# Kernel tuning notes

Hardware: AMD Instinct MI355X
Metric: run time of the kernel (lower is better)

The kernel has to match this reference:

```python
import jax, jax.numpy as jnp
import numpy as np

B = 8192
K = 40          # history blocks of 61
STATS = 383     # 99 base + 120 + 10 + 150 + 4 option dims
D = 165 + 61 * K + STATS  # 2988


def _mha(q, k, v, kpm, w_in, b_in, w_out, b_out, nh=4):
    """PyTorch nn.MultiheadAttention (batch_first) math. kpm: True = masked key."""
    Bq, Lq, E = q.shape
    hd = E // nh
    wq, wk, wv = jnp.split(w_in, 3, axis=0)
    bq, bk, bv = jnp.split(b_in, 3)
    qh = (q @ wq.T + bq).reshape(Bq, Lq, nh, hd).transpose(0, 2, 1, 3)
    kh = (k @ wk.T + bk).reshape(Bq, -1, nh, hd).transpose(0, 2, 1, 3)
    vh = (v @ wv.T + bv).reshape(Bq, -1, nh, hd).transpose(0, 2, 1, 3)
    s = jnp.einsum('bhqd,bhkd->bhqk', qh, kh) * jnp.float32(1.0 / np.sqrt(hd))
    if kpm is not None:
        s = jnp.where(kpm[:, None, None, :], jnp.float32(-1e9), s)
    a = jax.nn.softmax(s, axis=-1)
    o = jnp.einsum('bhqk,bhkd->bhqd', a, vh).transpose(0, 2, 1, 3).reshape(Bq, Lq, E)
    return o @ w_out.T + b_out


def _ln(x, g, b, eps=1e-5):
    m = x.mean(-1, keepdims=True)
    v = ((x - m) ** 2).mean(-1, keepdims=True)
    return (x - m) / jnp.sqrt(v + eps) * g + b


def setup_inputs() -> dict:
    key = jax.random.key(0)
    ks = iter(jax.random.split(key, 64))
    def p(shape, scale=0.02):
        return jax.random.normal(next(ks), shape, dtype=jnp.float32) * scale
    return {
        'obs': jax.random.normal(next(ks), (B, D), dtype=jnp.float32),
        'seat_team_vec': jax.random.normal(next(ks), (B, 6), dtype=jnp.float32),
        'card_emb': p((40, 32)),
        'w_cnt_hand': p((16, 3)), 'b_cnt_hand': p((16,)),
        'w_cnt_cap': p((16, 2)), 'b_cnt_cap': p((16,)),
        'h2t_win': p((96, 32)), 'h2t_bin': p((96,)), 'h2t_wout': p((32, 32)), 'h2t_bout': p((32,)),
        't2h_win': p((96, 32)), 't2h_bin': p((96,)), 't2h_wout': p((32, 32)), 't2h_bout': p((32,)),
        'w_merge': p((64, 224)), 'b_merge': p((64,)),
        'w_hproj': p((64, 61)), 'b_hproj': p((64,)),
        'pos_emb': p((40, 64)),
        'enc_win': p((192, 64)), 'enc_bin': p((192,)), 'enc_wout': p((64, 64)), 'enc_bout': p((64,)),
        'ln1_g': jnp.ones((64,), jnp.float32), 'ln1_b': jnp.zeros((64,), jnp.float32),
        'w_ff1': p((128, 64)), 'b_ff1': p((128,)),
        'w_ff2': p((64, 128)), 'b_ff2': p((64,)),
        'ln2_g': jnp.ones((64,), jnp.float32), 'ln2_b': jnp.zeros((64,), jnp.float32),
        'w_stats': p((64, STATS)), 'b_stats': p((64,)),
        'w_seat': p((32, 6)), 'b_seat': p((32,)),
        'w_comb': p((256, 224)), 'b_comb': p((256,)),
    }


def reference(obs, seat_team_vec, card_emb, w_cnt_hand, b_cnt_hand, w_cnt_cap, b_cnt_cap,
              h2t_win, h2t_bin, h2t_wout, h2t_bout, t2h_win, t2h_bin, t2h_wout, t2h_bout,
              w_merge, b_merge, w_hproj, b_hproj, pos_emb,
              enc_win, enc_bin, enc_wout, enc_bout, ln1_g, ln1_b,
              w_ff1, b_ff1, w_ff2, b_ff2, ln2_g, ln2_b,
              w_stats, b_stats, w_seat, b_seat, w_comb, b_comb):
    Bn = obs.shape[0]
    k = K  # static: decoded from D = 165 + 61*K + STATS
    hand_table = obs[:, :83]
    captured = obs[:, 83:165]
    history = obs[:, 165:165 + 61 * k]
    stats = obs[:, 165 + 61 * k:]

    hand_mask = hand_table[:, :40]
    other_counts = hand_table[:, 40:43]
    table_mask = hand_table[:, 43:83]

    hand_feat = hand_mask @ card_emb      # [B,32]
    table_feat = table_mask @ card_emb
    other_cnt_feat = jax.nn.relu(other_counts @ w_cnt_hand.T + b_cnt_hand)

    hand_present = hand_mask > 0.5
    table_present = table_mask > 0.5
    hand_seq = hand_mask[:, :, None] * card_emb    # [B,40,32]
    table_seq = table_mask[:, :, None] * card_emb

    # _safe_mha: rows whose keys are all padded produce zeros
    h2t = _mha(hand_seq, table_seq, table_seq, ~table_present, h2t_win, h2t_bin, h2t_wout, h2t_bout)
    h2t = jnp.where(table_present.any(axis=1)[:, None, None], h2t, jnp.float32(0.0))
    t2h = _mha(table_seq, hand_seq, hand_seq, ~hand_present, t2h_win, t2h_bin, t2h_wout, t2h_bout)
    t2h = jnp.where(hand_present.any(axis=1)[:, None, None], t2h, jnp.float32(0.0))

    def masked_mean(x, present):
        m = present[:, :, None].astype(x.dtype)
        return (x * m).sum(1) / jnp.maximum(m.sum(1), 1.0)
    hand_attn_feat = masked_mean(h2t, hand_present)
    table_attn_feat = masked_mean(t2h, table_present)

    cap0_feat = captured[:, :40] @ card_emb
    cap1_feat = captured[:, 40:80] @ card_emb
    cap_cnt_feat = jax.nn.relu(captured[:, 80:82] @ w_cnt_cap.T + b_cnt_cap)

    set_merged = jnp.concatenate([hand_feat, table_feat, cap0_feat, cap1_feat,
                                  hand_attn_feat, table_attn_feat,
                                  other_cnt_feat, cap_cnt_feat], axis=1)  # [B,224]
    set_feat = jax.nn.relu(set_merged @ w_merge.T + b_merge)              # [B,64]

    # 1-layer post-norm TransformerEncoder (eval mode, no dropout)
    hseq = history.reshape(Bn, k, 61) @ w_hproj.T + b_hproj + pos_emb[:k]  # [B,k,64]
    sa = _mha(hseq, hseq, hseq, None, enc_win, enc_bin, enc_wout, enc_bout)
    x = _ln(hseq + sa, ln1_g, ln1_b)
    ff = jax.nn.relu(x @ w_ff1.T + b_ff1) @ w_ff2.T + b_ff2
    x = _ln(x + ff, ln2_g, ln2_b)
    hist_feat = x.mean(axis=1)                                            # [B,64]

    stats_feat = jax.nn.relu(stats @ w_stats.T + b_stats)                 # [B,64]
    seat_feat = jax.nn.relu(seat_team_vec @ w_seat.T + b_seat)            # [B,32]

    combined = jnp.concatenate([set_feat, hist_feat, stats_feat, seat_feat], axis=1)  # [B,224]
    return jax.nn.relu(combined @ w_comb.T + b_comb)                      # [B,256]
```

## Files before the change

### kernel.cpp

```cpp
#include <hip/hip_runtime.h>

#define TPB 512

#define OFF_CV      0
#define OFF_POSB    2560
#define OFF_G       3840
#define OFF_U       10240
#define OFF_V       10560
#define OFF_CTB     10880
#define OFF_FRHP    10888
#define OFF_FRAG    14984
#define FR_QKV      0
#define FR_OUT      12288
#define FR_FF1      16384
#define FR_FF2      24576
#define OFF_MERGE   47752
#define OFF_STATS   62088
#define OFF_COMB    86600
#define OFF_WO2     143944
#define WS_TOTAL    144968

#define SA_OFF    0
#define HISTH_OFF 10240
#define HISTL_OFF 16768
#define QPL_OFF   10240
#define KF_OFF    16384
#define KZ_OFF    22528
#define OH_OFF    10240
#define FF1P_OFF  10240
#define C_OFF     23296
#define DH_OFF    33536
#define DL_OFF    40448
#define S_OFF     33536
#define SHT_OFF   47360
#define SOM_OFF   48032
#define SSM_OFF   48288
#define SCB_OFF   49184
#define R12_OFF   50208
#define SCNT_OFF  52256
#define SMEM_BYTES 52264

typedef __attribute__((ext_vector_type(8))) short bf16x8;
typedef __attribute__((ext_vector_type(4))) float f32x4;

struct P {
  const float *obs, *seat, *ce, *wch, *bch, *wcc, *bcc,
    *h2t_win, *h2t_bin, *h2t_wout, *h2t_bout,
    *t2h_win, *t2h_bin, *t2h_wout, *t2h_bout,
    *w_merge, *b_merge, *w_hproj, *b_hproj, *pos,
    *enc_win, *enc_bin, *enc_wout, *enc_bout,
    *ln1_g, *ln1_b, *w_ff1, *b_ff1, *w_ff2, *b_ff2, *ln2_g, *ln2_b,
    *w_stats, *b_stats, *w_seat, *b_seat, *w_comb, *b_comb;
  const float* ws;
  float* out;
};

__device__ __host__ inline unsigned bfpack(float a, float b, int plane) {
  unsigned ua = __float_as_uint(a) & 0xFFFF0000u;
  unsigned ub = __float_as_uint(b) & 0xFFFF0000u;
  if (plane == 0) return (ua >> 16) | ub;
  float ra = a - __uint_as_float(ua), rb = b - __uint_as_float(ub);
  return (__float_as_uint(ra) >> 16) | (__float_as_uint(rb) & 0xFFFF0000u);
}

__device__ inline unsigned short bf16rne(float x) {
  unsigned u = __float_as_uint(x);
  return (unsigned short)((u + 0x7FFFu + ((u >> 16) & 1u)) >> 16);
}

__device__ inline unsigned packrne(float a, float b) {
  return (unsigned)bf16rne(a) | ((unsigned)bf16rne(b) << 16);
}

__device__ inline float bf_lo(unsigned u) { return __uint_as_float(u << 16); }
__device__ inline float bf_hi(unsigned u) { return __uint_as_float(u & 0xFFFF0000u); }

__device__ inline bf16x8 ld_b64x2(const char* pp) {
  bf16x8 v;
  *((uint2*)&v) = *(const uint2*)(pp);
  *(((uint2*)&v) + 1) = *(const uint2*)(pp + 8);
  return v;
}

#define CSCALE 0.35355339059327373f

__global__ void prep_kernel(P p, float* ws) {
  int t = blockIdx.x * blockDim.x + threadIdx.x;
  if (t >= WS_TOTAL) return;
  unsigned* wsu = (unsigned*)ws;
  if (t < OFF_POSB) {
    int a = t / 1280, rem = t - a * 1280;
    int i = rem >> 5, d = rem & 31;
    const float* win = a ? p.t2h_win : p.h2t_win;
    const float* wr = win + (64 + d) * 32;
    const float* cr = p.ce + i * 32;
    float acc = 0.f;
    #pragma unroll
    for (int j = 0; j < 32; ++j) acc += cr[j] * wr[j];
    ws[t] = acc;
  } else if (t < OFF_G) {
    int r = t - OFF_POSB; int i = r >> 5, u = r & 31;
    float a = p.b_hproj[2 * u] + p.pos[i * 64 + 2 * u];
    float b = p.b_hproj[2 * u + 1] + p.pos[i * 64 + 2 * u + 1];
    wsu[t] = packrne(a, b);
  } else if (t < OFF_U) {
    int r = t - OFF_G;
    int u = r % 20; int i = (r / 20) % 40; int h = (r / 800) & 3; int a = r / 3200;
    const float* win = a ? p.t2h_win : p.h2t_win;
    const float* cri = p.ce + i * 32;
    float g2[2];
    #pragma unroll
    for (int half = 0; half < 2; ++half) {
      int j = 2 * u + half;
      const float* crj = p.ce + j * 32;
      float g = 0.f;
      for (int e = 0; e < 8; ++e) {
        const float* wq = win + (h * 8 + e) * 32;
        const float* wk = win + (32 + h * 8 + e) * 32;
        float pq = 0.f, pk = 0.f;
        for (int m = 0; m < 32; ++m) { pq += cri[m] * wq[m]; pk += crj[m] * wk[m]; }
        g += pq * pk;
      }
      g2[half] = g * CSCALE;
    }
    wsu[t] = packrne(g2[0], g2[1]);
  } else if (t < OFF_V) {
    int r = t - OFF_U; int i = r % 40; int h = (r / 40) & 3; int a = r / 160;
    const float* win = a ? p.t2h_win : p.h2t_win;
    const float* bin = a ? p.t2h_bin : p.h2t_bin;
    const float* cri = p.ce + i * 32;
    float u = 0.f;
    for (int e = 0; e < 8; ++e) {
      const float* wq = win + (h * 8 + e) * 32;
      float pq = 0.f;
      for (int m = 0; m < 32; ++m) pq += cri[m] * wq[m];
      u += pq * bin[32 + h * 8 + e];
    }
    ws[t] = u * CSCALE;
  } else if (t < OFF_CTB) {
    int r = t - OFF_V; int j = r % 40; int h = (r / 40) & 3; int a = r / 160;
    const float* win = a ? p.t2h_win : p.h2t_win;
    const float* bin = a ? p.t2h_bin : p.h2t_bin;
    const float* crj = p.ce + j * 32;
    float v = 0.f;
    for (int e = 0; e < 8; ++e) {
      const float* wk = win + (32 + h * 8 + e) * 32;
      float pk = 0.f;
      for (int m = 0; m < 32; ++m) pk += crj[m] * wk[m];
      v += pk * bin[h * 8 + e];
    }
    ws[t] = v * CSCALE;
  } else if (t < OFF_FRHP) {
    int r = t - OFF_CTB; int h = r & 3; int a = r >> 2;
    const float* bin = a ? p.t2h_bin : p.h2t_bin;
    float c = 0.f;
    for (int e = 0; e < 8; ++e) c += bin[h * 8 + e] * bin[32 + h * 8 + e];
    ws[t] = c * CSCALE;
  } else if (t < OFF_FRAG) {
    int r = t - OFF_FRHP;
    int plane = r >> 11; r &= 2047; int kt = r >> 10; r &= 1023;
    int nt = r >> 8; r &= 255; int lane = r >> 2; int u = r & 3;
    int k = kt * 32 + (lane >> 4) * 8 + u * 2;
    int n = nt * 16 + (lane & 15);
    float a = (k < 61) ? p.w_hproj[n * 61 + k] : 0.f;
    float b = (k + 1 < 61) ? p.w_hproj[n * 61 + k + 1] : 0.f;
    wsu[t] = bfpack(a, b, plane);
  } else if (t < OFF_MERGE) {
    int r = t - OFF_FRAG;
    int plane, kt, nt, lane, u;
    const float* src; int ldk;
    if (r < FR_OUT) {
      plane = r / 6144; r %= 6144; kt = r / 3072; r %= 3072;
      nt = r >> 8; r &= 255; lane = r >> 2; u = r & 3;
      src = p.enc_win; ldk = 64;
    } else if (r < FR_FF1) {
      r -= FR_OUT; plane = r >> 11; r &= 2047; kt = r >> 10; r &= 1023;
      nt = r >> 8; r &= 255; lane = r >> 2; u = r & 3;
      src = p.enc_wout; ldk = 64;
    } else if (r < FR_FF2) {
      r -= FR_FF1; plane = r >> 12; r &= 4095; kt = r >> 11; r &= 2047;
      nt = r >> 8; r &= 255; lane = r >> 2; u = r & 3;
      src = p.w_ff1; ldk = 64;
    } else {
      r -= FR_FF2; plane = r >> 12; r &= 4095; kt = r >> 10; r &= 1023;
      nt = r >> 8; r &= 255; lane = r >> 2; u = r & 3;
      src = p.w_ff2; ldk = 128;
    }
    int k = kt * 32 + (lane >> 4) * 8 + u * 2;
    int n = nt * 16 + (lane & 15);
    float a = src[n * ldk + k], b = src[n * ldk + k + 1];
    wsu[t] = bfpack(a, b, plane);
  } else if (t < OFF_STATS) {
    int r = t - OFF_MERGE; int j = r >> 6, d = r & 63;
    ws[t] = p.w_merge[d * 224 + j];
  } else if (t < OFF_COMB) {
    int r = t - OFF_STATS; int j = r >> 6, d = r & 63;
    ws[t] = p.w_stats[d * 383 + j];
  } else if (t < OFF_WO2) {
    int r = t - OFF_COMB; int j = r >> 8, d = r & 255;
    ws[t] = p.w_comb[d * 224 + j];
  } else {
    int r = t - OFF_WO2; int a = r >> 9; int rr = r & 511;
    int e = rr >> 4, u = rr & 15;
    const float* src = a ? p.t2h_wout : p.h2t_wout;
    wsu[t] = packrne(src[(2 * u) * 32 + e], src[(2 * u + 1) * 32 + e]);
  }
}

#define FMA4(acc, a4, w0, w1, w2, w3)                                   \
  acc.x += a4.x * w0.x + a4.y * w1.x + a4.z * w2.x + a4.w * w3.x;       \
  acc.y += a4.x * w0.y + a4.y * w1.y + a4.z * w2.y + a4.w * w3.y;       \
  acc.z += a4.x * w0.z + a4.y * w1.z + a4.z * w2.z + a4.w * w3.z;       \
  acc.w += a4.x * w0.w + a4.y * w1.w + a4.z * w2.w + a4.w * w3.w;

#define MFMA16(acc, a, b) acc = __builtin_amdgcn_mfma_f32_16x16x32_bf16(a, b, acc, 0, 0, 0)

__global__ __launch_bounds__(TPB, 3) void enc_row(P p) {
  const int row = blockIdx.x;
  const int tid = threadIdx.x;
  const int lane = tid & 63, wq = tid >> 6;
  const int lane15 = lane & 15, lg = lane >> 4;

  __shared__ unsigned smem_u[SMEM_BYTES / 4];
  char* smem = (char*)smem_u;
  float* sA   = (float*)(smem + SA_OFF);
  float* sC   = (float*)(smem + C_OFF);
  float* s_ht = (float*)(smem + SHT_OFF);
  float* s_om = (float*)(smem + SOM_OFF);
  float* s_sm = (float*)(smem + SSM_OFF);
  float* s_cb = (float*)(smem + SCB_OFF);
  float* s_r12 = (float*)(smem + R12_OFF);
  int*   s_cnt = (int*)(smem + SCNT_OFF);

  const float* orow = p.obs + (size_t)row * 2988;
  const float* ws = p.ws;
  const unsigned* wsu = (const unsigned*)ws;

  if (tid < 165) s_ht[tid] = orow[tid];
  if (tid < 32) {
    float a = 0.f;
    for (int i = 0; i < 40; ++i) a += orow[i] * p.ce[i * 32 + tid];
    s_sm[tid] = a;
  } else if (tid < 64) {
    int d = tid - 32; float a = 0.f;
    for (int i = 0; i < 40; ++i) a += orow[43 + i] * p.ce[i * 32 + d];
    s_sm[32 + d] = a;
  } else if (tid < 96) {
    int d = tid - 64; float a = 0.f;
    for (int i = 0; i < 40; ++i) a += orow[83 + i] * p.ce[i * 32 + d];
    s_sm[64 + d] = a;
  } else if (tid < 128) {
    int d = tid - 96; float a = 0.f;
    for (int i = 0; i < 40; ++i) a += orow[123 + i] * p.ce[i * 32 + d];
    s_sm[96 + d] = a;
  } else if (tid < 144) {
    int d = tid - 128;
    float a = p.bch[d];
    for (int j = 0; j < 3; ++j) a += orow[40 + j] * p.wch[d * 3 + j];
    s_sm[192 + d] = fmaxf(a, 0.f);
  } else if (tid < 160) {
    int d = tid - 144;
    float a = p.bcc[d];
    for (int j = 0; j < 2; ++j) a += orow[163 + j] * p.wcc[d * 2 + j];
    s_sm[208 + d] = fmaxf(a, 0.f);
  }
  if (tid >= 192 && tid < 256) s_om[tid - 192] = 0.f;
  if (tid >= 256 && tid < 320) s_cb[128 + tid - 256] = p.b_stats[tid - 256];
  if (tid >= 384 && tid < 448) s_cb[tid - 384] = p.b_merge[tid - 384];
  if (tid == 320) {
    int c = 0; for (int i = 0; i < 40; ++i) c += (orow[i] > 0.5f);
    s_cnt[0] = c;
  } else if (tid == 321) {
    int c = 0; for (int i = 0; i < 40; ++i) c += (orow[43 + i] > 0.5f);
    s_cnt[1] = c;
  }
  if (tid >= 448) {
    int z = tid - 448;
    ((unsigned*)(smem + KZ_OFF))[z] = 0u;
    ((unsigned*)(smem + KZ_OFF))[z + 64] = 0u;
  }
  for (int m = tid; m < 2560; m += TPB) {
    int i = m >> 6, j = m & 63;
    float val = (j < 61) ? orow[165 + i * 61 + j] : 0.f;
    unsigned hb = __float_as_uint(val) & 0xFFFF0000u;
    *(unsigned short*)(smem + HISTH_OFF + i * 136 + j * 2) = (unsigned short)(hb >> 16);
    float rr = val - __uint_as_float(hb);
    *(unsigned short*)(smem + HISTL_OFF + i * 136 + j * 2) =
        (unsigned short)(__float_as_uint(rr) >> 16);
  }
  __syncthreads();
  #define OB(i) s_ht[i]

  for (int t = wq; t < 12; t += 8) {
    int rt = t % 3, nt = t / 3;
    int n = nt * 16 + lane15;
    int arow = rt * 16 + lane15;
    f32x4 acc;
    #pragma unroll
    for (int r = 0; r < 4; ++r) {
      int i = rt * 16 + lg * 4 + r;
      if (i < 40) {
        unsigned pb = wsu[OFF_POSB + i * 32 + (n >> 1)];
        acc[r] = (n & 1) ? bf_hi(pb) : bf_lo(pb);
      } else acc[r] = 0.f;
    }
    #pragma unroll
    for (int kt = 0; kt < 2; ++kt) {
      int kb = kt * 32 + lg * 8;
      bf16x8 aH = ld_b64x2(smem + HISTH_OFF + arow * 136 + kb * 2);
      bf16x8 aL = ld_b64x2(smem + HISTL_OFF + arow * 136 + kb * 2);
      bf16x8 bH = *(const bf16x8*)(wsu + OFF_FRHP + kt * 1024 + nt * 256 + lane * 4);
      bf16x8 bL = *(const bf16x8*)(wsu + OFF_FRHP + 2048 + kt * 1024 + nt * 256 + lane * 4);
      MFMA16(acc, aH, bH); MFMA16(acc, aH, bL); MFMA16(acc, aL, bH);
    }
    #pragma unroll
    for (int r = 0; r < 4; ++r) {
      int i = rt * 16 + lg * 4 + r;
      if (i < 40) {
        sA[i * 64 + n] = acc[r];
        unsigned hb = __float_as_uint(acc[r]) & 0xFFFF0000u;
        *(unsigned short*)(smem + DH_OFF + i * 144 + n * 2) = (unsigned short)(hb >> 16);
        float rr = acc[r] - __uint_as_float(hb);
        *(unsigned short*)(smem + DL_OFF + i * 144 + n * 2) =
            (unsigned short)(__float_as_uint(rr) >> 16);
      }
    }
  }
  if (tid < 320) {
    int a = tid / 160, r = tid - a * 160;
    int h = r / 40, i = r - h * 40;
    int qoff = a ? 43 : 0, koff = a ? 0 : 43;
    float qm = OB(qoff + i);
    const unsigned* Gp = wsu + OFF_G + ((a * 4 + h) * 40 + i) * 20;
    const float* vp = ws + OFF_V + (a * 4 + h) * 40;
    const float* Cv = ws + OFF_CV + a * 1280;
    const float* bin = a ? p.t2h_bin : p.h2t_bin;
    float base = ws[OFF_CTB + a * 4 + h] + qm * ws[OFF_U + (a * 4 + h) * 40 + i];
    const int e0 = h * 8;
    float den = 0.f;
    float o0 = 0.f, o1 = 0.f, o2 = 0.f, o3 = 0.f;
    float o4 = 0.f, o5 = 0.f, o6 = 0.f, o7 = 0.f;
    for (int j = 0; j < 40; ++j) {
      float km = OB(koff + j);
      if (km > 0.5f) {
        unsigned g2 = Gp[j >> 1];
        float gj = (j & 1) ? bf_hi(g2) : bf_lo(g2);
        float s = fmaf(km, fmaf(qm, gj, vp[j]), base);
        float pj = __expf(s);
        den += pj;
        float pk = pj * km;
        float4 v0 = *(const float4*)(Cv + j * 32 + e0);
        float4 v1 = *(const float4*)(Cv + j * 32 + e0 + 4);
        o0 += pk * v0.x; o1 += pk * v0.y; o2 += pk * v0.z; o3 += pk * v0.w;
        o4 += pk * v1.x; o5 += pk * v1.y; o6 += pk * v1.z; o7 += pk * v1.w;
      }
    }
    if (qm > 0.5f) {
      float inv = 1.f / den;
      float4 bv0 = *(const float4*)(bin + 64 + e0);
      float4 bv1 = *(const float4*)(bin + 64 + e0 + 4);
      atomicAdd(&s_om[a * 32 + e0 + 0], o0 * inv + bv0.x);
      atomicAdd(&s_om[a * 32 + e0 + 1], o1 * inv + bv0.y);
      atomicAdd(&s_om[a * 32 + e0 + 2], o2 * inv + bv0.z);
      atomicAdd(&s_om[a * 32 + e0 + 3], o3 * inv + bv0.w);
      atomicAdd(&s_om[a * 32 + e0 + 4], o4 * inv + bv1.x);
      atomicAdd(&s_om[a * 32 + e0 + 5], o5 * inv + bv1.y);
      atomicAdd(&s_om[a * 32 + e0 + 6], o6 * inv + bv1.z);
      atomicAdd(&s_om[a * 32 + e0 + 7], o7 * inv + bv1.w);
    }
  } else {
    int r = tid - 320;
    int c = r >> 4, d0 = (r & 15) << 2;
    int j0 = c << 5, j1 = (c == 11) ? 383 : j0 + 32;
    const float* st = orow + 2605;
    const float* wt = ws + OFF_STATS + d0;
    float x0 = 0.f, x1 = 0.f, x2 = 0.f, x3 = 0.f;
    for (int j = j0; j < j1; ++j) {
      float a0 = st[j];
      float4 w = *(const float4*)(wt + j * 64);
      x0 += a0 * w.x; x1 += a0 * w.y; x2 += a0 * w.z; x3 += a0 * w.w;
    }
    atomicAdd(&s_cb[128 + d0 + 0], x0);
    atomicAdd(&s_cb[128 + d0 + 1], x1);
    atomicAdd(&s_cb[128 + d0 + 2], x2);
    atomicAdd(&s_cb[128 + d0 + 3], x3);
  }
  __syncthreads();

  for (int t = wq; t < 36; t += 8) {
    int rt = t % 3, nt = t / 3;
    int n = nt * 16 + lane15;
    int arow = rt * 16 + lane15;
    float bia = p.enc_bin[n];
    f32x4 acc = {bia, bia, bia, bia};
    #pragma unroll
    for (int kt = 0; kt < 2; ++kt) {
      int kb = kt * 32 + lg * 8;
      bf16x8 aH = *(const bf16x8*)(smem + DH_OFF + arow * 144 + kb * 2);
      bf16x8 aL = *(const bf16x8*)(smem + DL_OFF + arow * 144 + kb * 2);
      bf16x8 bH = *(const bf16x8*)(wsu + OFF_FRAG + FR_QKV + kt * 3072 + nt * 256 + lane * 4);
      bf16x8 bL = *(const bf16x8*)(wsu + OFF_FRAG + FR_QKV + 6144 + kt * 3072 + nt * 256 + lane * 4);
      MFMA16(acc, aH, bH); MFMA16(acc, aH, bL); MFMA16(acc, aL, bH);
    }
    if (nt < 4) {
      #pragma unroll
      for (int r = 0; r < 4; ++r) {
        int i = rt * 16 + lg * 4 + r;
        if (i < 40)
          *(unsigned short*)(smem + QPL_OFF + ((nt * 48 + i) * 16 + lane15) * 2) =
              bf16rne(acc[r]);
      }
    } else if (nt < 8) {
      int h = nt - 4, e = lane15;
      int lp = (e >> 3) << 4, us = e & 7;
      #pragma unroll
      for (int r = 0; r < 4; ++r) {
        int j = rt * 16 + lg * 4 + r;
        if (j < 40) {
          int lanep = lp + (j & 15);
          *(unsigned short*)(smem + KF_OFF +
              (((h * 3 + (j >> 4)) * 32 + lanep) * 8 + us) * 2) = bf16rne(acc[r]);
        }
      }
    } else {
      int col = n - 128;
      #pragma unroll
      for (int r = 0; r < 4; ++r) {
        int i = rt * 16 + lg * 4 + r;
        if (i < 40) sC[i * 64 + col] = acc[r];
      }
    }
  }
  if (tid < 16) {
    int a = tid >> 3, d0 = (tid & 7) << 2;
    int ch = s_cnt[0], ct = s_cnt[1];
    float4 v = make_float4(0.f, 0.f, 0.f, 0.f);
    if (ch > 0 && ct > 0) {
      float ic = 1.f / (float)(a ? ct : ch);
      const unsigned* wt = wsu + OFF_WO2 + a * 512 + (d0 >> 1);
      const float* om = s_om + a * 32;
      v = *(const float4*)((a ? p.t2h_bout : p.h2t_bout) + d0);
      for (int e = 0; e < 32; ++e) {
        float oe = om[e] * ic;
        unsigned w01 = wt[e * 16], w23 = wt[e * 16 + 1];
        v.x += oe * bf_lo(w01); v.y += oe * bf_hi(w01);
        v.z += oe * bf_lo(w23); v.w += oe * bf_hi(w23);
      }
    }
    *(float4*)(s_sm + 128 + a * 32 + d0) = v;
  }
  __syncthreads();

  for (int t = wq; t < 36; t += 8) {
    int h = t / 9, rr = t % 9;
    int rt = rr / 3, nt = rr % 3;
    int arow = rt * 16 + lane15;
    f32x4 acc = {0.f, 0.f, 0.f, 0.f};
    bf16x8 aH = *(const bf16x8*)(smem + QPL_OFF + ((h * 48 + arow) * 16 + (lg & 1) * 8) * 2);
    int boff = (lane < 32) ? (KF_OFF + (((h * 3 + nt) * 32 + lane) * 8) * 2)
                           : (KZ_OFF + ((lane & 31) * 8) * 2);
    bf16x8 bH = *(const bf16x8*)(smem + boff);
    MFMA16(acc, aH, bH);
    int j = nt * 16 + lane15;
    #pragma unroll
    for (int r = 0; r < 4; ++r) {
      int i = rt * 16 + lg * 4 + r;
      if (i < 40 && j < 40)
        *(unsigned short*)(smem + S_OFF + ((h * 40 + i) * 42 + j) * 2) =
            bf16rne(acc[r] * 0.25f);
    }
  }
  __syncthreads();

  if (tid < 320) {
    int eh = tid & 1, q = tid >> 1;
    int h = q / 40, i = q - h * 40;
    const int e0 = h * 16 + eh * 8;
    const unsigned short* Sp = (const unsigned short*)(smem + S_OFF) + (h * 40 + i) * 42;
    float den = 0.f;
    float o8[8];
    #pragma unroll
    for (int e = 0; e < 8; ++e) o8[e] = 0.f;
    for (int j = 0; j < 40; ++j) {
      float s = __uint_as_float(((unsigned)Sp[j]) << 16);
      float pj = __expf(s);
      den += pj;
      const float* vr = sC + (j << 6) + e0;
      float4 v0 = *(const float4*)vr;
      float4 v1 = *(const float4*)(vr + 4);
      o8[0] += pj * v0.x; o8[1] += pj * v0.y; o8[2] += pj * v0.z; o8[3] += pj * v0.w;
      o8[4] += pj * v1.x; o8[5] += pj * v1.y; o8[6] += pj * v1.z; o8[7] += pj * v1.w;
    }
    float inv = 1.f / den;
    #pragma unroll
    for (int m = 0; m < 4; ++m) {
      unsigned h2 = packrne(o8[2 * m] * inv, o8[2 * m + 1] * inv);
      *(unsigned*)(smem + OH_OFF + i * 144 + (e0 + 2 * m) * 2) = h2;
    }
  } else if (tid < 384) {
    int r = tid - 320;
    int d0 = (r & 15) << 2, jq = r >> 4;
    const float* wt = ws + OFF_MERGE + d0;
    float4 acc = make_float4(0.f, 0.f, 0.f, 0.f);
    int j0 = jq * 56;
    for (int j = j0; j < j0 + 56; j += 4) {
      float4 a4 = *(const float4*)(s_sm + j);
      float4 w0 = *(const float4*)(wt + j * 64);
      float4 w1 = *(const float4*)(wt + (j + 1) * 64);
      float4 w2 = *(const float4*)(wt + (j + 2) * 64);
      float4 w3 = *(const float4*)(wt + (j + 3) * 64);
      FMA4(acc, a4, w0, w1, w2, w3);
    }
    atomicAdd(&s_cb[d0 + 0], acc.x);
    atomicAdd(&s_cb[d0 + 1], acc.y);
    atomicAdd(&s_cb[d0 + 2], acc.z);
    atomicAdd(&s_cb[d0 + 3], acc.w);
  }
  __syncthreads();

  for (int t = wq; t < 12; t += 8) {
    int rt = t % 3, nt = t / 3;
    int n = nt * 16 + lane15;
    int arow = rt * 16 + lane15;
    f32x4 acc;
    #pragma unroll
    for (int r = 0; r < 4; ++r) {
      int i = rt * 16 + lg * 4 + r;
      acc[r] = p.enc_bout[n] + ((i < 40) ? sA[i * 64 + n] : 0.f);
    }
    #pragma unroll
    for (int kt = 0; kt < 2; ++kt) {
      int kb = kt * 32 + lg * 8;
      bf16x8 aH = *(const bf16x8*)(smem + OH_OFF + arow * 144 + kb * 2);
      bf16x8 bH = *(const bf16x8*)(wsu + OFF_FRAG + FR_OUT + kt * 1024 + nt * 256 + lane * 4);
      bf16x8 bL = *(const bf16x8*)(wsu + OFF_FRAG + FR_OUT + 2048 + kt * 1024 + nt * 256 + lane * 4);
      MFMA16(acc, aH, bH); MFMA16(acc, aH, bL);
    }
    #pragma unroll
    for (int r = 0; r < 4; ++r) {
      int i = rt * 16 + lg * 4 + r;
      if (i < 40) sC[i * 64 + n] = acc[r];
    }
  }
  __syncthreads();

  {
    float g = p.ln1_g[lane], b = p.ln1_b[lane];
    for (int i = wq; i < 40; i += 8) {
      float x = sC[(i << 6) + lane];
      float s = x;
      #pragma unroll
      for (int off = 32; off; off >>= 1) s += __shfl_xor(s, off, 64);
      float m = s * 0.015625f;
      float xm = x - m;
      float v = xm * xm;
      #pragma unroll
      for (int off = 32; off; off >>= 1) v += __shfl_xor(v, off, 64);
      float rs = rsqrtf(v * 0.015625f + 1e-5f);
      float val = xm * rs * g + b;
      sA[(i << 6) + lane] = val;
      unsigned hb = __float_as_uint(val) & 0xFFFF0000u;
      *(unsigned short*)(smem + DH_OFF + i * 144 + lane * 2) = (unsigned short)(hb >> 16);
      float rr = val - __uint_as_float(hb);
      *(unsigned short*)(smem + DL_OFF + i * 144 + lane * 2) =
          (unsigned short)(__float_as_uint(rr) >> 16);
    }
  }
  __syncthreads();

  for (int t = wq; t < 24; t += 8) {
    int rt = t % 3, nt = t / 3;
    int n = nt * 16 + lane15;
    int arow = rt * 16 + lane15;
    float bia = p.b_ff1[n];
    f32x4 acc = {bia, bia, bia, bia};
    #pragma unroll
    for (int kt = 0; kt < 2; ++kt) {
      int kb = kt * 32 + lg * 8;
      bf16x8 aH = *(const bf16x8*)(smem + DH_OFF + arow * 144 + kb * 2);
      bf16x8 aL = *(const bf16x8*)(smem + DL_OFF + arow * 144 + kb * 2);
      bf16x8 bH = *(const bf16x8*)(wsu + OFF_FRAG + FR_FF1 + kt * 2048 + nt * 256 + lane * 4);
      bf16x8 bL = *(const bf16x8*)(wsu + OFF_FRAG + FR_FF1 + 4096 + kt * 2048 + nt * 256 + lane * 4);
      MFMA16(acc, aH, bH); MFMA16(acc, aH, bL); MFMA16(acc, aL, bH);
    }
    #pragma unroll
    for (int r = 0; r < 4; ++r) {
      int i = rt * 16 + lg * 4 + r;
      float v = fmaxf(acc[r], 0.f);
      *(unsigned short*)(smem + FF1P_OFF + i * 272 + n * 2) = bf16rne(v);
    }
  }
  __syncthreads();

  for (int t = wq; t < 12; t += 8) {
    int rt = t % 3, nt = t / 3;
    int n = nt * 16 + lane15;
    int arow = rt * 16 + lane15;
    f32x4 acc;
    #pragma unroll
    for (int r = 0; r < 4; ++r) {
      int i = rt * 16 + lg * 4 + r;
      acc[r] = p.b_ff2[n] + ((i < 40) ? sA[i * 64 + n] : 0.f);
    }
    #pragma unroll
    for (int kt = 0; kt < 4; ++kt) {
      int kb = kt * 32 + lg * 8;
      bf16x8 aH = *(const bf16x8*)(smem + FF1P_OFF + arow * 272 + kb * 2);
      bf16x8 bH = *(const bf16x8*)(wsu + OFF_FRAG + FR_FF2 + kt * 1024 + nt * 256 + lane * 4);
      bf16x8 bL = *(const bf16x8*)(wsu + OFF_FRAG + FR_FF2 + 4096 + kt * 1024 + nt * 256 + lane * 4);
      MFMA16(acc, aH, bH); MFMA16(acc, aH, bL);
    }
    #pragma unroll
    for (int r = 0; r < 4; ++r) {
      int i = rt * 16 + lg * 4 + r;
      if (i < 40) sC[i * 64 + n] = acc[r];
    }
  }
  __syncthreads();

  {
    float g = p.ln2_g[lane], b = p.ln2_b[lane];
    for (int i = wq; i < 40; i += 8) {
      float x = sC[(i << 6) + lane];
      float s = x;
      #pragma unroll
      for (int off = 32; off; off >>= 1) s += __shfl_xor(s, off, 64);
      float m = s * 0.015625f;
      float xm = x - m;
      float v = xm * xm;
      #pragma unroll
      for (int off = 32; off; off >>= 1) v += __shfl_xor(v, off, 64);
      float rs = rsqrtf(v * 0.015625f + 1e-5f);
      sA[(i << 6) + lane] = xm * rs * g + b;
    }
  }
  __syncthreads();

  if (tid < 64) {
    float a = 0.f;
    for (int i = 0; i < 40; ++i) a += sA[(i << 6) + tid];
    s_cb[64 + tid] = a * 0.025f;
    s_cb[128 + tid] = fmaxf(s_cb[128 + tid], 0.f);
    s_cb[tid] = fmaxf(s_cb[tid], 0.f);
  } else if (tid < 96) {
    int d = tid - 64;
    const float* sv = p.seat + (size_t)row * 6;
    float acc = p.b_seat[d];
    for (int j = 0; j < 6; ++j) acc += sv[j] * p.w_seat[d * 6 + j];
    s_cb[192 + d] = fmaxf(acc, 0.f);
  }
  __syncthreads();

  {
    int n = tid & 255, half = tid >> 8;
    const float* wt = ws + OFF_COMB + n;
    float acc = half ? 0.f : p.b_comb[n];
    int j0 = half * 112;
    for (int j = j0; j < j0 + 112; j += 4) {
      float4 a4 = *(const float4*)(s_cb + j);
      acc += a4.x * wt[j * 256] + a4.y * wt[(j + 1) * 256]
           + a4.z * wt[(j + 2) * 256] + a4.w * wt[(j + 3) * 256];
    }
    s_r12[half * 256 + n] = acc;
  }
  __syncthreads();
  if (tid < 256)
    p.out[(size_t)row * 256 + tid] = fmaxf(s_r12[tid] + s_r12[256 + tid], 0.f);
  #undef OB
}

extern "C" void kernel_launch(void* const* d_in, const int* in_sizes, int n_in,
                              void* d_out, int out_size, void* d_ws, size_t ws_size,
                              hipStream_t stream) {
  typedef const float* F;
  P p;
  p.obs      = (F)d_in[0];
  p.seat     = (F)d_in[1];
  p.ce       = (F)d_in[2];
  p.wch      = (F)d_in[3];
  p.bch      = (F)d_in[4];
  p.wcc      = (F)d_in[5];
  p.bcc      = (F)d_in[6];
  p.h2t_win  = (F)d_in[7];
  p.h2t_bin  = (F)d_in[8];
  p.h2t_wout = (F)d_in[9];
  p.h2t_bout = (F)d_in[10];
  p.t2h_win  = (F)d_in[11];
  p.t2h_bin  = (F)d_in[12];
  p.t2h_wout = (F)d_in[13];
  p.t2h_bout = (F)d_in[14];
  p.w_merge  = (F)d_in[15];
  p.b_merge  = (F)d_in[16];
  p.w_hproj  = (F)d_in[17];
  p.b_hproj  = (F)d_in[18];
  p.pos      = (F)d_in[19];
  p.enc_win  = (F)d_in[20];
  p.enc_bin  = (F)d_in[21];
  p.enc_wout = (F)d_in[22];
  p.enc_bout = (F)d_in[23];
  p.ln1_g    = (F)d_in[24];
  p.ln1_b    = (F)d_in[25];
  p.w_ff1    = (F)d_in[26];
  p.b_ff1    = (F)d_in[27];
  p.w_ff2    = (F)d_in[28];
  p.b_ff2    = (F)d_in[29];
  p.ln2_g    = (F)d_in[30];
  p.ln2_b    = (F)d_in[31];
  p.w_stats  = (F)d_in[32];
  p.b_stats  = (F)d_in[33];
  p.w_seat   = (F)d_in[34];
  p.b_seat   = (F)d_in[35];
  p.w_comb   = (F)d_in[36];
  p.b_comb   = (F)d_in[37];
  p.ws  = (const float*)d_ws;
  p.out = (float*)d_out;

  const int Bn = in_sizes[0] / 2988;
  hipLaunchKernelGGL(prep_kernel, dim3((WS_TOTAL + 255) / 256), dim3(256), 0, stream,
                     p, (float*)d_ws);
  hipLaunchKernelGGL(enc_row, dim3(Bn), dim3(TPB), 0, stream, p);
}
```

Measured before the change: 864.8 us.

## Move encoder softmax-V product to MFMA and reduce atomic contention

Replaces the scalar per-thread softmax·V loop with MFMA: exponentiated scores go to shared memory as bf16, V is stored in fragment layout, and a ones-matrix MFMA produces the denominators. Stats weights are packed to bf16, the comb weights are re-laid out for float4 loads, and the card embedding and output-projection work is split across more threads. Shared-memory atomics are spread over two accumulation banks, and the cross-attention constant is copied into shared memory. The bf16 rounding of exp scores and stats weights lowers precision, and the added zero-fill passes add setup work.

```diff
diff --git a/kernel.cpp b/kernel.cpp
--- a/kernel.cpp
+++ b/kernel.cpp
@@ -14,11 +14,12 @@
 #define FR_OUT      12288
 #define FR_FF1      16384
 #define FR_FF2      24576
-#define OFF_MERGE   47752
-#define OFF_STATS   62088
-#define OFF_COMB    86600
-#define OFF_WO2     143944
-#define WS_TOTAL    144968
+#define OFF_ONES    47752
+#define OFF_MERGE   48264
+#define OFF_STATS   62600
+#define OFF_COMB    74856
+#define OFF_WO2     132200
+#define WS_TOTAL    133224
 
 #define SA_OFF    0
 #define HISTH_OFF 10240
@@ -28,17 +29,19 @@
 #define KZ_OFF    22528
 #define OH_OFF    10240
 #define FF1P_OFF  10240
-#define C_OFF     23296
-#define DH_OFF    33536
-#define DL_OFF    40448
-#define S_OFF     33536
+#define DH_OFF    23296
+#define DL_OFF    30208
+#define P_OFF     23296
+#define YTAIL_OFF 36096
+#define Z_OFF     37120
+#define VF_OFF    37120
 #define SHT_OFF   47360
 #define SOM_OFF   48032
-#define SSM_OFF   48288
-#define SCB_OFF   49184
-#define R12_OFF   50208
-#define SCNT_OFF  52256
-#define SMEM_BYTES 52264
+#define SSM_OFF   48544
+#define SCB_OFF   49440
+#define R12_OFF   50464
+#define SCNT_OFF  52512
+#define SMEM_BYTES 52520
 
 typedef __attribute__((ext_vector_type(8))) short bf16x8;
 typedef __attribute__((ext_vector_type(4))) float f32x4;
@@ -63,12 +66,12 @@
   return (__float_as_uint(ra) >> 16) | (__float_as_uint(rb) & 0xFFFF0000u);
 }
 
-__device__ inline unsigned short bf16rne(float x) {
+__device__ __host__ inline unsigned short bf16rne(float x) {
   unsigned u = __float_as_uint(x);
   return (unsigned short)((u + 0x7FFFu + ((u >> 16) & 1u)) >> 16);
 }
 
-__device__ inline unsigned packrne(float a, float b) {
+__device__ __host__ inline unsigned packrne(float a, float b) {
   return (unsigned)bf16rne(a) | ((unsigned)bf16rne(b) << 16);
 }
 
@@ -165,7 +168,7 @@
     float a = (k < 61) ? p.w_hproj[n * 61 + k] : 0.f;
     float b = (k + 1 < 61) ? p.w_hproj[n * 61 + k + 1] : 0.f;
     wsu[t] = bfpack(a, b, plane);
-  } else if (t < OFF_MERGE) {
+  } else if (t < OFF_ONES) {
     int r = t - OFF_FRAG;
     int plane, kt, nt, lane, u;
     const float* src; int ldk;
@@ -190,15 +193,24 @@
     int n = nt * 16 + (lane & 15);
     float a = src[n * ldk + k], b = src[n * ldk + k + 1];
     wsu[t] = bfpack(a, b, plane);
+  } else if (t < OFF_MERGE) {
+    int r = t - OFF_ONES;
+    int kt = r >> 8, rr = r & 255;
+    int lane = rr >> 2, u = rr & 3;
+    int k = kt * 32 + (lane >> 4) * 8 + u * 2;
+    wsu[t] = ((k < 40) ? 0x00003F80u : 0u) | ((k + 1 < 40) ? 0x3F800000u : 0u);
   } else if (t < OFF_STATS) {
     int r = t - OFF_MERGE; int j = r >> 6, d = r & 63;
     ws[t] = p.w_merge[d * 224 + j];
   } else if (t < OFF_COMB) {
-    int r = t - OFF_STATS; int j = r >> 6, d = r & 63;
-    ws[t] = p.w_stats[d * 383 + j];
+    int r = t - OFF_STATS;
+    int j = r >> 5, pp = r & 31;
+    wsu[t] = packrne(p.w_stats[(2 * pp) * 383 + j], p.w_stats[(2 * pp + 1) * 383 + j]);
   } else if (t < OFF_WO2) {
-    int r = t - OFF_COMB; int j = r >> 8, d = r & 255;
-    ws[t] = p.w_comb[d * 224 + j];
+    int r = t - OFF_COMB;
+    int jq = r >> 10, rem = r & 1023;
+    int n = rem >> 2, c = rem & 3;
+    ws[t] = p.w_comb[n * 224 + jq * 4 + c];
   } else {
     int r = t - OFF_WO2; int a = r >> 9; int rr = r & 511;
     int e = rr >> 4, u = rr & 15;
@@ -224,7 +236,7 @@
   __shared__ unsigned smem_u[SMEM_BYTES / 4];
   char* smem = (char*)smem_u;
   float* sA   = (float*)(smem + SA_OFF);
-  float* sC   = (float*)(smem + C_OFF);
+  float* sZ   = (float*)(smem + Z_OFF);
   float* s_ht = (float*)(smem + SHT_OFF);
   float* s_om = (float*)(smem + SOM_OFF);
   float* s_sm = (float*)(smem + SSM_OFF);
@@ -237,48 +249,42 @@
   const unsigned* wsu = (const unsigned*)ws;
 
   if (tid < 165) s_ht[tid] = orow[tid];
-  if (tid < 32) {
+  if (tid < 256) ((unsigned*)(smem + YTAIL_OFF))[tid] = 0u;
+  if (tid < 256) {
+    int feat = tid >> 6, q = tid & 63;
+    int d = q >> 1, jh = q & 1;
+    const int offs[4] = {0, 43, 83, 123};
+    const int dsts[4] = {0, 32, 64, 96};
+    int off = offs[feat];
     float a = 0.f;
-    for (int i = 0; i < 40; ++i) a += orow[i] * p.ce[i * 32 + tid];
-    s_sm[tid] = a;
-  } else if (tid < 64) {
-    int d = tid - 32; float a = 0.f;
-    for (int i = 0; i < 40; ++i) a += orow[43 + i] * p.ce[i * 32 + d];
-    s_sm[32 + d] = a;
-  } else if (tid < 96) {
-    int d = tid - 64; float a = 0.f;
-    for (int i = 0; i < 40; ++i) a += orow[83 + i] * p.ce[i * 32 + d];
-    s_sm[64 + d] = a;
-  } else if (tid < 128) {
-    int d = tid - 96; float a = 0.f;
-    for (int i = 0; i < 40; ++i) a += orow[123 + i] * p.ce[i * 32 + d];
-    s_sm[96 + d] = a;
-  } else if (tid < 144) {
-    int d = tid - 128;
+    for (int j = jh * 20; j < jh * 20 + 20; ++j)
+      a += orow[off + j] * p.ce[j * 32 + d];
+    float other = __shfl_xor(a, 1, 64);
+    if (jh == 0) s_sm[dsts[feat] + d] = a + other;
+  } else if (tid < 272) {
+    int d = tid - 256;
     float a = p.bch[d];
     for (int j = 0; j < 3; ++j) a += orow[40 + j] * p.wch[d * 3 + j];
     s_sm[192 + d] = fmaxf(a, 0.f);
-  } else if (tid < 160) {
-    int d = tid - 144;
+  } else if (tid < 288) {
+    int d = tid - 272;
     float a = p.bcc[d];
     for (int j = 0; j < 2; ++j) a += orow[163 + j] * p.wcc[d * 2 + j];
     s_sm[208 + d] = fmaxf(a, 0.f);
-  }
-  if (tid >= 192 && tid < 256) s_om[tid - 192] = 0.f;
-  if (tid >= 256 && tid < 320) s_cb[128 + tid - 256] = p.b_stats[tid - 256];
-  if (tid >= 384 && tid < 448) s_cb[tid - 384] = p.b_merge[tid - 384];
-  if (tid == 320) {
+  } else if (tid < 352) {
+    s_sm[128 + tid - 288] = 0.f;
+  } else if (tid < 480) {
+    s_om[tid - 352] = 0.f;
+  } else if (tid == 480) {
     int c = 0; for (int i = 0; i < 40; ++i) c += (orow[i] > 0.5f);
     s_cnt[0] = c;
-  } else if (tid == 321) {
+  } else if (tid == 481) {
     int c = 0; for (int i = 0; i < 40; ++i) c += (orow[43 + i] > 0.5f);
     s_cnt[1] = c;
   }
-  if (tid >= 448) {
-    int z = tid - 448;
-    ((unsigned*)(smem + KZ_OFF))[z] = 0u;
-    ((unsigned*)(smem + KZ_OFF))[z + 64] = 0u;
-  }
+  if (tid < 64) s_cb[128 + tid] = p.b_stats[tid];
+  else if (tid < 128) s_cb[tid - 64] = p.b_merge[tid - 64];
+  else if (tid < 256) s_r12[tid - 128] = 0.f;
   for (int m = tid; m < 2560; m += TPB) {
     int i = m >> 6, j = m & 63;
     float val = (j < 61) ? orow[165 + i * 61 + j] : 0.f;
@@ -288,6 +294,7 @@
     *(unsigned short*)(smem + HISTL_OFF + i * 136 + j * 2) =
         (unsigned short)(__float_as_uint(rr) >> 16);
   }
+  for (int m = tid; m < 2560; m += TPB) sZ[m] = ws[OFF_CV + m];
   __syncthreads();
   #define OB(i) s_ht[i]
 
@@ -333,7 +340,7 @@
     float qm = OB(qoff + i);
     const unsigned* Gp = wsu + OFF_G + ((a * 4 + h) * 40 + i) * 20;
     const float* vp = ws + OFF_V + (a * 4 + h) * 40;
-    const float* Cv = ws + OFF_CV + a * 1280;
+    const float* Cv = sZ + a * 1280;
     const float* bin = a ? p.t2h_bin : p.h2t_bin;
     float base = ws[OFF_CTB + a * 4 + h] + qm * ws[OFF_U + (a * 4 + h) * 40 + i];
     const int e0 = h * 8;
@@ -359,31 +366,34 @@
       float inv = 1.f / den;
       float4 bv0 = *(const float4*)(bin + 64 + e0);
       float4 bv1 = *(const float4*)(bin + 64 + e0 + 4);
-      atomicAdd(&s_om[a * 32 + e0 + 0], o0 * inv + bv0.x);
-      atomicAdd(&s_om[a * 32 + e0 + 1], o1 * inv + bv0.y);
-      atomicAdd(&s_om[a * 32 + e0 + 2], o2 * inv + bv0.z);
-      atomicAdd(&s_om[a * 32 + e0 + 3], o3 * inv + bv0.w);
-      atomicAdd(&s_om[a * 32 + e0 + 4], o4 * inv + bv1.x);
-      atomicAdd(&s_om[a * 32 + e0 + 5], o5 * inv + bv1.y);
-      atomicAdd(&s_om[a * 32 + e0 + 6], o6 * inv + bv1.z);
-      atomicAdd(&s_om[a * 32 + e0 + 7], o7 * inv + bv1.w);
+      float* om = s_om + (i & 1) * 64 + a * 32 + e0;
+      atomicAdd(&om[0], o0 * inv + bv0.x);
+      atomicAdd(&om[1], o1 * inv + bv0.y);
+      atomicAdd(&om[2], o2 * inv + bv0.z);
+      atomicAdd(&om[3], o3 * inv + bv0.w);
+      atomicAdd(&om[4], o4 * inv + bv1.x);
+      atomicAdd(&om[5], o5 * inv + bv1.y);
+      atomicAdd(&om[6], o6 * inv + bv1.z);
+      atomicAdd(&om[7], o7 * inv + bv1.w);
     }
   } else {
     int r = tid - 320;
     int c = r >> 4, d0 = (r & 15) << 2;
     int j0 = c << 5, j1 = (c == 11) ? 383 : j0 + 32;
     const float* st = orow + 2605;
-    const float* wt = ws + OFF_STATS + d0;
+    const unsigned* wt = wsu + OFF_STATS + (d0 >> 1);
     float x0 = 0.f, x1 = 0.f, x2 = 0.f, x3 = 0.f;
     for (int j = j0; j < j1; ++j) {
       float a0 = st[j];
-      float4 w = *(const float4*)(wt + j * 64);
-      x0 += a0 * w.x; x1 += a0 * w.y; x2 += a0 * w.z; x3 += a0 * w.w;
-    }
-    atomicAdd(&s_cb[128 + d0 + 0], x0);
-    atomicAdd(&s_cb[128 + d0 + 1], x1);
-    atomicAdd(&s_cb[128 + d0 + 2], x2);
-    atomicAdd(&s_cb[128 + d0 + 3], x3);
+      unsigned u0 = wt[j * 32], u1 = wt[j * 32 + 1];
+      x0 += a0 * bf_lo(u0); x1 += a0 * bf_hi(u0);
+      x2 += a0 * bf_lo(u1); x3 += a0 * bf_hi(u1);
+    }
+    float* bank = (c & 1) ? s_r12 : (s_cb + 128);
+    atomicAdd(&bank[d0 + 0], x0);
+    atomicAdd(&bank[d0 + 1], x1);
+    atomicAdd(&bank[d0 + 2], x2);
+    atomicAdd(&bank[d0 + 3], x3);
   }
   __syncthreads();
 
@@ -423,31 +433,45 @@
         }
       }
     } else {
-      int col = n - 128;
+      int h = nt - 8, e = lane15;
       #pragma unroll
       for (int r = 0; r < 4; ++r) {
-        int i = rt * 16 + lg * 4 + r;
-        if (i < 40) sC[i * 64 + col] = acc[r];
-      }
-    }
-  }
-  if (tid < 16) {
-    int a = tid >> 3, d0 = (tid & 7) << 2;
+        int j = rt * 16 + lg * 4 + r;
+        if (j < 40) {
+          int kt = j >> 5, k_ = j & 31;
+          int lanep = ((k_ >> 3) << 4) | e;
+          *(unsigned short*)(smem + VF_OFF +
+              (((h * 2 + kt) * 64 + lanep) * 8 + (k_ & 7)) * 2) = bf16rne(acc[r]);
+        }
+      }
+    }
+  }
+  if (tid < 128) ((unsigned*)(smem + KZ_OFF))[tid] = 0u;
+  for (int m = tid; m < 768; m += TPB) {
+    int h = m / 192, rem = m - h * 192;
+    ((unsigned*)(smem + VF_OFF))[(h * 2 + 1) * 256 + 64 + rem] = 0u;
+  }
+  if (tid >= 448 && tid < 480) {
+    int r = tid - 448;
+    int a = r >> 4, q = r & 15;
+    int d0 = (q >> 1) << 2, eh = q & 1;
     int ch = s_cnt[0], ct = s_cnt[1];
-    float4 v = make_float4(0.f, 0.f, 0.f, 0.f);
     if (ch > 0 && ct > 0) {
       float ic = 1.f / (float)(a ? ct : ch);
       const unsigned* wt = wsu + OFF_WO2 + a * 512 + (d0 >> 1);
-      const float* om = s_om + a * 32;
-      v = *(const float4*)((a ? p.t2h_bout : p.h2t_bout) + d0);
-      for (int e = 0; e < 32; ++e) {
-        float oe = om[e] * ic;
+      float4 v = make_float4(0.f, 0.f, 0.f, 0.f);
+      if (eh == 0) v = *(const float4*)((a ? p.t2h_bout : p.h2t_bout) + d0);
+      for (int e = eh * 16; e < eh * 16 + 16; ++e) {
+        float oe = (s_om[a * 32 + e] + s_om[64 + a * 32 + e]) * ic;
         unsigned w01 = wt[e * 16], w23 = wt[e * 16 + 1];
         v.x += oe * bf_lo(w01); v.y += oe * bf_hi(w01);
         v.z += oe * bf_lo(w23); v.w += oe * bf_hi(w23);
       }
-    }
-    *(float4*)(s_sm + 128 + a * 32 + d0) = v;
+      atomicAdd(&s_sm[128 + a * 32 + d0 + 0], v.x);
+      atomicAdd(&s_sm[128 + a * 32 + d0 + 1], v.y);
+      atomicAdd(&s_sm[128 + a * 32 + d0 + 2], v.z);
+      atomicAdd(&s_sm[128 + a * 32 + d0 + 3], v.w);
+    }
   }
   __syncthreads();
 
@@ -462,48 +486,51 @@
     bf16x8 bH = *(const bf16x8*)(smem + boff);
     MFMA16(acc, aH, bH);
     int j = nt * 16 + lane15;
-    #pragma unroll
-    for (int r = 0; r < 4; ++r) {
-      int i = rt * 16 + lg * 4 + r;
-      if (i < 40 && j < 40)
-        *(unsigned short*)(smem + S_OFF + ((h * 40 + i) * 42 + j) * 2) =
-            bf16rne(acc[r] * 0.25f);
-    }
-  }
-  __syncthreads();
-
-  if (tid < 320) {
-    int eh = tid & 1, q = tid >> 1;
-    int h = q / 40, i = q - h * 40;
-    const int e0 = h * 16 + eh * 8;
-    const unsigned short* Sp = (const unsigned short*)(smem + S_OFF) + (h * 40 + i) * 42;
-    float den = 0.f;
-    float o8[8];
-    #pragma unroll
-    for (int e = 0; e < 8; ++e) o8[e] = 0.f;
-    for (int j = 0; j < 40; ++j) {
-      float s = __uint_as_float(((unsigned)Sp[j]) << 16);
-      float pj = __expf(s);
-      den += pj;
-      const float* vr = sC + (j << 6) + e0;
-      float4 v0 = *(const float4*)vr;
-      float4 v1 = *(const float4*)(vr + 4);
-      o8[0] += pj * v0.x; o8[1] += pj * v0.y; o8[2] += pj * v0.z; o8[3] += pj * v0.w;
-      o8[4] += pj * v1.x; o8[5] += pj * v1.y; o8[6] += pj * v1.z; o8[7] += pj * v1.w;
-    }
-    float inv = 1.f / den;
-    #pragma unroll
-    for (int m = 0; m < 4; ++m) {
-      unsigned h2 = packrne(o8[2 * m] * inv, o8[2 * m + 1] * inv);
-      *(unsigned*)(smem + OH_OFF + i * 144 + (e0 + 2 * m) * 2) = h2;
-    }
-  } else if (tid < 384) {
-    int r = tid - 320;
-    int d0 = (r & 15) << 2, jq = r >> 4;
+    if (j < 40) {
+      #pragma unroll
+      for (int r = 0; r < 4; ++r) {
+        int i = rt * 16 + lg * 4 + r;
+        if (i < 40)
+          *(unsigned short*)(smem + P_OFF + h * 3200 + i * 80 + j * 2) =
+              bf16rne(__expf(acc[r] * 0.25f));
+      }
+    }
+  }
+  __syncthreads();
+
+  {
+    bf16x8 ones0 = *(const bf16x8*)(wsu + OFF_ONES + lane * 4);
+    bf16x8 ones1 = *(const bf16x8*)(wsu + OFF_ONES + 256 + lane * 4);
+    for (int t = wq; t < 12; t += 8) {
+      int h = t / 3, rt = t % 3;
+      int arow = rt * 16 + lane15;
+      const char* pb = smem + P_OFF + h * 3200 + arow * 80;
+      bf16x8 a0 = *(const bf16x8*)(pb + lg * 16);
+      bf16x8 a1 = {0, 0, 0, 0, 0, 0, 0, 0};
+      if (lg == 0) a1 = *(const bf16x8*)(pb + 64);
+      bf16x8 v0 = *(const bf16x8*)(smem + VF_OFF + ((h * 2 + 0) * 64 + lane) * 16);
+      bf16x8 v1 = *(const bf16x8*)(smem + VF_OFF + ((h * 2 + 1) * 64 + lane) * 16);
+      f32x4 accV = {0.f, 0.f, 0.f, 0.f}, accD = {0.f, 0.f, 0.f, 0.f};
+      MFMA16(accV, a0, v0); MFMA16(accV, a1, v1);
+      MFMA16(accD, a0, ones0); MFMA16(accD, a1, ones1);
+      #pragma unroll
+      for (int r = 0; r < 4; ++r) {
+        int i = rt * 16 + lg * 4 + r;
+        if (i < 40) {
+          float o = accV[r] / accD[r];
+          *(unsigned short*)(smem + OH_OFF + (i * 72 + h * 16 + lane15) * 2) =
+              bf16rne(o);
+        }
+      }
+    }
+  }
+  if (tid >= 256 && tid < 384) {
+    int r = tid - 256;
+    int d0 = (r & 15) << 2, jc = r >> 4;
     const float* wt = ws + OFF_MERGE + d0;
     float4 acc = make_float4(0.f, 0.f, 0.f, 0.f);
-    int j0 = jq * 56;
-    for (int j = j0; j < j0 + 56; j += 4) {
+    int j0 = jc * 28;
+    for (int j = j0; j < j0 + 28; j += 4) {
       float4 a4 = *(const float4*)(s_sm + j);
       float4 w0 = *(const float4*)(wt + j * 64);
       float4 w1 = *(const float4*)(wt + (j + 1) * 64);
@@ -511,10 +538,11 @@
       float4 w3 = *(const float4*)(wt + (j + 3) * 64);
       FMA4(acc, a4, w0, w1, w2, w3);
     }
-    atomicAdd(&s_cb[d0 + 0], acc.x);
-    atomicAdd(&s_cb[d0 + 1], acc.y);
-    atomicAdd(&s_cb[d0 + 2], acc.z);
-    atomicAdd(&s_cb[d0 + 3], acc.w);
+    float* bank = (jc & 1) ? (s_r12 + 64) : s_cb;
+    atomicAdd(&bank[d0 + 0], acc.x);
+    atomicAdd(&bank[d0 + 1], acc.y);
+    atomicAdd(&bank[d0 + 2], acc.z);
+    atomicAdd(&bank[d0 + 3], acc.w);
   }
   __syncthreads();
 
@@ -539,7 +567,7 @@
     #pragma unroll
     for (int r = 0; r < 4; ++r) {
       int i = rt * 16 + lg * 4 + r;
-      if (i < 40) sC[i * 64 + n] = acc[r];
+      if (i < 40) sZ[i * 64 + n] = acc[r];
     }
   }
   __syncthreads();
@@ -547,7 +575,7 @@
   {
     float g = p.ln1_g[lane], b = p.ln1_b[lane];
     for (int i = wq; i < 40; i += 8) {
-      float x = sC[(i << 6) + lane];
+      float x = sZ[(i << 6) + lane];
       float s = x;
       #pragma unroll
       for (int off = 32; off; off >>= 1) s += __shfl_xor(s, off, 64);
@@ -613,7 +641,7 @@
     #pragma unroll
     for (int r = 0; r < 4; ++r) {
       int i = rt * 16 + lg * 4 + r;
-      if (i < 40) sC[i * 64 + n] = acc[r];
+      if (i < 40) sZ[i * 64 + n] = acc[r];
     }
   }
   __syncthreads();
@@ -621,7 +649,7 @@
   {
     float g = p.ln2_g[lane], b = p.ln2_b[lane];
     for (int i = wq; i < 40; i += 8) {
-      float x = sC[(i << 6) + lane];
+      float x = sZ[(i << 6) + lane];
       float s = x;
       #pragma unroll
       for (int off = 32; off; off >>= 1) s += __shfl_xor(s, off, 64);
@@ -640,8 +668,8 @@
     float a = 0.f;
     for (int i = 0; i < 40; ++i) a += sA[(i << 6) + tid];
     s_cb[64 + tid] = a * 0.025f;
-    s_cb[128 + tid] = fmaxf(s_cb[128 + tid], 0.f);
-    s_cb[tid] = fmaxf(s_cb[tid], 0.f);
+    s_cb[128 + tid] = fmaxf(s_cb[128 + tid] + s_r12[tid], 0.f);
+    s_cb[tid] = fmaxf(s_cb[tid] + s_r12[64 + tid], 0.f);
   } else if (tid < 96) {
     int d = tid - 64;
     const float* sv = p.seat + (size_t)row * 6;
@@ -653,13 +681,13 @@
 
   {
     int n = tid & 255, half = tid >> 8;
-    const float* wt = ws + OFF_COMB + n;
+    const float* wt = ws + OFF_COMB + n * 4;
     float acc = half ? 0.f : p.b_comb[n];
-    int j0 = half * 112;
-    for (int j = j0; j < j0 + 112; j += 4) {
-      float4 a4 = *(const float4*)(s_cb + j);
-      acc += a4.x * wt[j * 256] + a4.y * wt[(j + 1) * 256]
-           + a4.z * wt[(j + 2) * 256] + a4.w * wt[(j + 3) * 256];
+    int jq0 = half * 28;
+    for (int jq = jq0; jq < jq0 + 28; ++jq) {
+      float4 a4 = *(const float4*)(s_cb + jq * 4);
+      float4 w = *(const float4*)(wt + jq * 1024);
+      acc += a4.x * w.x + a4.y * w.y + a4.z * w.z + a4.w * w.w;
     }
     s_r12[half * 256 + n] = acc;
   }
```

New measurement: 825.4 us. 1.05x faster.
